# Performance work log

Measured on AMD Instinct MI355X. Metric: run time of the kernel, lower is better.

The kernel has to match this reference:

```python
import jax, jax.numpy as jnp
import numpy as np

B, C, H, W = 4, 512, 64, 64
CA = C // 2  # attention hidden channels


def _conv1x1(x, w):
    # w: [O, I], x: [B, I, H, W]
    return jnp.einsum('oi,bihw->bohw', w, x)


def _conv3x3(x, w, b):
    y = jax.lax.conv_general_dilated(x, w, (1, 1), 'SAME',
                                     dimension_numbers=('NCHW', 'OIHW', 'NCHW'))
    return y + b[None, :, None, None]


def _scan_dir(x, w, b, axis, reverse):
    # IRNN recurrence along `axis`: prev = relu(prev * w + b + x_t), per-channel w,b.
    # The boundary position (first in scan order after un-flipping) stays zero,
    # matching the torch code which never writes it.
    xs = jnp.moveaxis(x, axis, 0)          # [L, B, C, other]
    if reverse:
        xs = xs[::-1]
    wb = w.reshape(1, -1, 1)
    bb = b.reshape(1, -1, 1)

    def step(prev, xt):
        new = jax.nn.relu(prev * wb + bb + xt)
        return new, new

    init = jax.nn.relu(xs[0])
    _, ys = jax.lax.scan(step, init, xs[1:])
    ys = jnp.concatenate([jnp.zeros_like(ys[:1]), ys], axis=0)
    if reverse:
        ys = ys[::-1]
    return jnp.moveaxis(ys, 0, axis)


def _irnn(x, wu, wr, wd, wl, bu, br, bd, bl):
    up = _scan_dir(x, wu, bu, 2, True)     # scans from bottom row upward
    right = _scan_dir(x, wr, br, 3, False)
    down = _scan_dir(x, wd, bd, 2, False)
    left = _scan_dir(x, wl, bl, 3, True)
    return up, right, down, left


def setup_inputs() -> dict:
    key = jax.random.key(0)
    ks = jax.random.split(key, 32)

    def n(k, shape, scale):
        return jax.random.normal(k, shape, jnp.float32) * scale

    inp = {
        'x': n(ks[0], (B, C, H, W), 1.0),
        # Attention: conv3x3(C->C/2)+b, conv3x3(C/2->C/2)+b, conv1x1(C/2->4)+b
        'a_w1': n(ks[1], (CA, C, 3, 3), (C * 9) ** -0.5),
        'a_b1': n(ks[2], (CA,), 0.02),
        'a_w2': n(ks[3], (CA, CA, 3, 3), (CA * 9) ** -0.5),
        'a_b2': n(ks[4], (CA,), 0.02),
        'a_w3': n(ks[5], (4, CA, 1, 1), CA ** -0.5),
        'a_b3': n(ks[6], (4,), 0.02),
        'cin_w': n(ks[7], (C, C), C ** -0.5),   # conv_in 1x1, bias=False
        'c2_w': n(ks[8], (C, 4 * C), (4 * C) ** -0.5),
        'c3_w': n(ks[9], (C, 4 * C), (4 * C) ** -0.5),
    }
    # IRNN per-channel recurrence weights (alpha=1.0 init) and biases
    i = 10
    for tag in ('i1', 'i2'):
        for d in ('u', 'r', 'd', 'l'):
            inp[f'{tag}_w{d}'] = jnp.ones((C,), jnp.float32)
            inp[f'{tag}_b{d}'] = n(ks[i], (C,), 0.05)
            i += 1
    return inp


def reference(x, a_w1, a_b1, a_w2, a_b2, a_w3, a_b3, cin_w,
              i1_wu, i1_bu, i1_wr, i1_br, i1_wd, i1_bd, i1_wl, i1_bl,
              c2_w,
              i2_wu, i2_bu, i2_wr, i2_br, i2_wd, i2_bd, i2_wl, i2_bl,
              c3_w):
    # Attention branch — computed but NEVER applied: the original torch code
    # uses out-of-place .mul() and discards the result (faithful reproduction).
    a = jax.nn.relu(_conv3x3(x, a_w1, a_b1))
    a = jax.nn.relu(_conv3x3(a, a_w2, a_b2))
    _weight = jax.nn.sigmoid(_conv1x1(a, a_w3[:, :, 0, 0]) + a_b3[None, :, None, None])

    out = _conv1x1(x, cin_w)
    u, r, d, l = _irnn(out, i1_wu, i1_wr, i1_wd, i1_wl, i1_bu, i1_br, i1_bd, i1_bl)
    out = jnp.concatenate([u, r, d, l], axis=1)   # [B, 4C, H, W]
    out = _conv1x1(out, c2_w)
    u, r, d, l = _irnn(out, i2_wu, i2_wr, i2_wd, i2_wl, i2_bu, i2_br, i2_bd, i2_bl)
    out = jnp.concatenate([u, r, d, l], axis=1)
    out = jax.nn.relu(_conv1x1(out, c3_w))
    return out
```

## Files before the change

### kernel.cpp

```cpp
#include <hip/hip_runtime.h>
#include <stdint.h>

#define NB 4
#define CB 512
#define HH 64
#define WW 64
#define HW 4096
#define C4 2048
#define PTOT (NB*HW)

typedef float  f32x4  __attribute__((ext_vector_type(4)));
typedef short  bf16x8 __attribute__((ext_vector_type(8)));

__device__ __forceinline__ float relu_f(float v){ return v > 0.f ? v : 0.f; }

__device__ __forceinline__ float bf2f(unsigned short u){
    union { uint32_t i; float f; } v; v.i = ((uint32_t)u) << 16; return v.f;
}
__device__ __forceinline__ unsigned short f2bf(float f){
    union { float f; uint32_t i; } v; v.f = f;
    uint32_t r = v.i + 0x7FFFu + ((v.i >> 16) & 1u);
    return (unsigned short)(r >> 16);
}

__device__ __forceinline__ void gload16(const void* g, void* l){
    __builtin_amdgcn_global_load_lds(
        (const __attribute__((address_space(1))) uint32_t*)g,
        (__attribute__((address_space(3))) uint32_t*)l, 16, 0, 0);
}

__global__ __launch_bounds__(256) void cast3_f32_bf16(
    const float* __restrict__ a, unsigned short* __restrict__ oa,
    const float* __restrict__ b, unsigned short* __restrict__ ob,
    const float* __restrict__ c, unsigned short* __restrict__ oc)
{
    int i = blockIdx.x * 256 + threadIdx.x;
    const float* src; unsigned short* dst; int j;
    if (i < 65536)        { src = a; dst = oa; j = i; }
    else if (i < 327680)  { src = b; dst = ob; j = i - 65536; }
    else                  { src = c; dst = oc; j = i - 327680; }
    float4 v = ((const float4*)src)[j];
    ushort4 o;
    o.x = f2bf(v.x); o.y = f2bf(v.y); o.z = f2bf(v.z); o.w = f2bf(v.w);
    ((ushort4*)dst)[j] = o;
}

__global__ __launch_bounds__(256) void transpose_cast_x(
    const float* __restrict__ x, unsigned short* __restrict__ xT)
{
    __shared__ unsigned short tile[64][72];
    const int b  = blockIdx.z;
    const int p0 = blockIdx.x * 64;
    const int c0 = blockIdx.y * 64;
    const int t  = threadIdx.x;

    const int pl = (t & 15) * 4;
    const int cl = t >> 4;
    const float* src = x + ((size_t)b * CB + c0) * HW + p0;
    #pragma unroll
    for (int r = 0; r < 4; r++) {
        int c = cl + r * 16;
        float4 v = *(const float4*)(src + (size_t)c * HW + pl);
        tile[pl + 0][c] = f2bf(v.x);
        tile[pl + 1][c] = f2bf(v.y);
        tile[pl + 2][c] = f2bf(v.z);
        tile[pl + 3][c] = f2bf(v.w);
    }
    __syncthreads();
    unsigned short* dst = xT + ((size_t)b * HW + p0) * CB + c0;
    const int cl2 = (t & 15) * 4;
    const int pl2 = t >> 4;
    #pragma unroll
    for (int r = 0; r < 4; r++) {
        int p = pl2 + r * 16;
        ushort4 o = *(ushort4*)&tile[p][cl2];
        *(ushort4*)(dst + (size_t)p * CB + cl2) = o;
    }
}

template<int K, int OUTMODE>
__global__ __launch_bounds__(512) void gemm_cl(
    const unsigned short* __restrict__ A,
    const unsigned short* __restrict__ Bw,
    void* __restrict__ out)
{
    extern __shared__ __align__(16) char lds[];

    const int t    = threadIdx.x;
    const int lane = t & 63;
    const int wid  = t >> 6;
    const int p0   = blockIdx.x * 256;
    const int o0   = blockIdx.y * 128;

    const int l15 = lane & 15;
    const int l4  = lane >> 4;
    const int m0  = (wid >> 1) * 64;
    const int n0  = (wid & 1) * 64;
    const int swz = (l15 & 7) << 4;

    f32x4 acc[4][4];
    #pragma unroll
    for (int m = 0; m < 4; m++)
        #pragma unroll
        for (int n = 0; n < 4; n++) acc[m][n] = (f32x4)0.f;

    const int sr  = lane >> 3;
    const int scb = (lane & 7) * 16;
    const int skk = (scb ^ (sr << 4)) >> 1;

    auto STAGE_A = [&](int k0, int half, char* buf) {
        #pragma unroll
        for (int j = 0; j < 2; ++j) {
            const int r = half * 128 + j * 64 + wid * 8 + sr;
            gload16(A + (size_t)(p0 + r) * K + k0 + skk,
                    buf + half * 16384 + j * 8192 + wid * 1024);
        }
    };
    auto STAGE_B = [&](int k0, char* buf) {
        #pragma unroll
        for (int j = 0; j < 2; ++j) {
            const int r = j * 64 + wid * 8 + sr;
            gload16(Bw + (size_t)(o0 + r) * K + k0 + skk,
                    buf + 32768 + j * 8192 + wid * 1024);
        }
    };

    char* buf0 = lds;
    char* buf1 = lds + 49152;
    char* buf2 = lds + 98304;

    STAGE_A(0, 0, buf0); STAGE_A(0, 1, buf0); STAGE_B(0, buf0);
    STAGE_A(64, 0, buf1); STAGE_A(64, 1, buf1); STAGE_B(64, buf1);

    char* cur = buf0; char* nxt = buf1; char* fut = buf2;
    const int NT = K / 64;

#define PH(khv, mhv, STCODE)                                                   \
    {                                                                          \
        const int colb = (khv) * 64 + l4 * 16;                                 \
        af0 = *(const bf16x8*)(cur + (m0 + (2*(mhv)  )*16 + l15)*128 + (colb ^ swz)); \
        af1 = *(const bf16x8*)(cur + (m0 + (2*(mhv)+1)*16 + l15)*128 + (colb ^ swz)); \
        if ((mhv) == 0) {                                                      \
            _Pragma("unroll")                                                  \
            for (int nn = 0; nn < 4; ++nn)                                     \
                bfr[nn] = *(const bf16x8*)(cur + 32768 +                       \
                           (n0 + nn*16 + l15)*128 + (colb ^ swz));             \
        }                                                                      \
        STCODE;                                                                \
        __builtin_amdgcn_s_barrier();                                          \
        asm volatile("s_waitcnt lgkmcnt(0)" ::: "memory");                     \
        __builtin_amdgcn_sched_barrier(0);                                     \
        __builtin_amdgcn_s_setprio(1);                                         \
        _Pragma("unroll")                                                      \
        for (int nn = 0; nn < 4; ++nn) {                                       \
            acc[2*(mhv)  ][nn] = __builtin_amdgcn_mfma_f32_16x16x32_bf16(      \
                                    af0, bfr[nn], acc[2*(mhv)  ][nn], 0, 0, 0);\
            acc[2*(mhv)+1][nn] = __builtin_amdgcn_mfma_f32_16x16x32_bf16(      \
                                    af1, bfr[nn], acc[2*(mhv)+1][nn], 0, 0, 0);\
        }                                                                      \
        __builtin_amdgcn_s_setprio(0);                                         \
        __builtin_amdgcn_sched_barrier(0);                                     \
        __builtin_amdgcn_s_barrier();                                          \
    }

    for (int tt = 0; tt < NT; ++tt) {
        if (tt < NT - 1) asm volatile("s_waitcnt vmcnt(6)" ::: "memory");
        else             asm volatile("s_waitcnt vmcnt(0)" ::: "memory");
        __builtin_amdgcn_s_barrier();

        const int  k2 = (tt + 2) * 64;
        const bool st = (tt + 2 < NT);
        bf16x8 bfr[4], af0, af1;

        PH(0, 0, { if (st) STAGE_A(k2, 0, fut); })
        PH(0, 1, { if (st) STAGE_A(k2, 1, fut); })
        PH(1, 0, { if (st) STAGE_B(k2, fut);    })
        PH(1, 1, { })

        char* tmp = cur; cur = nxt; nxt = fut; fut = tmp;
    }
#undef PH

    if (OUTMODE == 0) {
        unsigned short* op = (unsigned short*)out;
        #pragma unroll
        for (int m = 0; m < 4; m++)
            #pragma unroll
            for (int r = 0; r < 4; r++) {
                const int p = p0 + m0 + m * 16 + l4 * 4 + r;
                #pragma unroll
                for (int n = 0; n < 4; n++) {
                    const int o = o0 + n0 + n * 16 + l15;
                    op[(size_t)p * CB + o] = f2bf(acc[m][n][r]);
                }
            }
    } else {
        __syncthreads();
        float (*tl)[260] = (float(*)[260])lds;
        #pragma unroll
        for (int n = 0; n < 4; n++)
            #pragma unroll
            for (int m = 0; m < 4; m++)
                #pragma unroll
                for (int r = 0; r < 4; r++)
                    tl[n0 + n * 16 + l15][m0 + m * 16 + l4 * 4 + r] = acc[m][n][r];
        __syncthreads();
        const int bb   = p0 >> 12;
        const int phw0 = p0 & (HW - 1);
        const int orow = t >> 2;
        const int pseg = (t & 3) * 64;
        float* dst = (float*)out + ((size_t)(bb * CB + o0 + orow)) * HW + phw0 + pseg;
        #pragma unroll
        for (int j = 0; j < 16; j++) {
            float4 v = *(float4*)&tl[orow][pseg + j * 4];
            v.x = relu_f(v.x); v.y = relu_f(v.y); v.z = relu_f(v.z); v.w = relu_f(v.w);
            *(float4*)(dst + j * 4) = v;
        }
    }
}

__global__ __launch_bounds__(256) void irnn_fused(
    const unsigned short* __restrict__ in, unsigned short* __restrict__ outc,
    const float* __restrict__ wu, const float* __restrict__ bu,
    const float* __restrict__ wr, const float* __restrict__ br,
    const float* __restrict__ wd, const float* __restrict__ bd,
    const float* __restrict__ wl, const float* __restrict__ bl)
{
    const int dir = blockIdx.y;
    const float* wv; const float* bv; int pstep, rev;
    if      (dir == 0) { wv = wu; bv = bu; pstep = 64; rev = 1; }
    else if (dir == 1) { wv = wr; bv = br; pstep = 1;  rev = 0; }
    else if (dir == 2) { wv = wd; bv = bd; pstep = 64; rev = 0; }
    else               { wv = wl; bv = bl; pstep = 1;  rev = 1; }
    const int dirOff = dir * 512;

    const int idx = blockIdx.x * 256 + threadIdx.x;
    const int c = idx & 511;
    const int f = (idx >> 9) & 63;
    const int b = idx >> 15;
    const int fbase = (pstep == 64) ? f : f * 64;

    const float wc = wv[c], bc = bv[c];
    const int t0 = rev ? 63 : 0;
    const int dp = rev ? -pstep : pstep;
    const int istep = dp * CB;
    const int ostep = dp * C4;

    const unsigned short* ip = in   + ((size_t)b * HW + fbase + (size_t)t0 * pstep) * CB + c;
    unsigned short*       op = outc + ((size_t)b * HW + fbase + (size_t)t0 * pstep) * C4 + dirOff + c;

    float s = relu_f(bf2f(ip[0]));
    op[0] = 0;

    unsigned short v0 = ip[1*istep], v1 = ip[2*istep], v2 = ip[3*istep], v3 = ip[4*istep],
                   v4 = ip[5*istep], v5 = ip[6*istep], v6 = ip[7*istep], v7 = ip[8*istep];

#define DO(kk, vv) { s = relu_f(fmaf(s, wc, bc + bf2f(vv))); op[(kk)*ostep] = f2bf(s); }
    for (int g = 0; g < 6; ++g) {
        const int k0 = 1 + 8 * g;
        DO(k0+0, v0); v0 = ip[(k0+ 8)*istep];
        DO(k0+1, v1); v1 = ip[(k0+ 9)*istep];
        DO(k0+2, v2); v2 = ip[(k0+10)*istep];
        DO(k0+3, v3); v3 = ip[(k0+11)*istep];
        DO(k0+4, v4); v4 = ip[(k0+12)*istep];
        DO(k0+5, v5); v5 = ip[(k0+13)*istep];
        DO(k0+6, v6); v6 = ip[(k0+14)*istep];
        DO(k0+7, v7); v7 = ip[(k0+15)*istep];
    }
    DO(49, v0); v0 = ip[57*istep];
    DO(50, v1); v1 = ip[58*istep];
    DO(51, v2); v2 = ip[59*istep];
    DO(52, v3); v3 = ip[60*istep];
    DO(53, v4); v4 = ip[61*istep];
    DO(54, v5); v5 = ip[62*istep];
    DO(55, v6); v6 = ip[63*istep];
    DO(56, v7);
    DO(57, v0); DO(58, v1); DO(59, v2); DO(60, v3);
    DO(61, v4); DO(62, v5); DO(63, v6);
#undef DO
}

extern "C" void kernel_launch(void* const* d_in, const int* in_sizes, int n_in,
                              void* d_out, int out_size, void* d_ws, size_t ws_size,
                              hipStream_t stream) {
    const float* x     = (const float*)d_in[0];
    const float* cin_w = (const float*)d_in[7];
    const float* c2_w  = (const float*)d_in[8];
    const float* c3_w  = (const float*)d_in[9];
    const float* i1_wu = (const float*)d_in[10];
    const float* i1_bu = (const float*)d_in[11];
    const float* i1_wr = (const float*)d_in[12];
    const float* i1_br = (const float*)d_in[13];
    const float* i1_wd = (const float*)d_in[14];
    const float* i1_bd = (const float*)d_in[15];
    const float* i1_wl = (const float*)d_in[16];
    const float* i1_bl = (const float*)d_in[17];
    const float* i2_wu = (const float*)d_in[18];
    const float* i2_bu = (const float*)d_in[19];
    const float* i2_wr = (const float*)d_in[20];
    const float* i2_br = (const float*)d_in[21];
    const float* i2_wd = (const float*)d_in[22];
    const float* i2_bd = (const float*)d_in[23];
    const float* i2_wl = (const float*)d_in[24];
    const float* i2_bl = (const float*)d_in[25];

    char* ws = (char*)d_ws;
    unsigned short* xT     = (unsigned short*)(ws);
    unsigned short* concat = (unsigned short*)(ws + (size_t)16 * 1024 * 1024);
    unsigned short* mid    = (unsigned short*)(ws + (size_t)80 * 1024 * 1024);
    unsigned short* wA     = (unsigned short*)(ws + (size_t)96 * 1024 * 1024);
    unsigned short* wB     = (unsigned short*)(wA + 512 * 512);
    unsigned short* wC     = (unsigned short*)(wB + 512 * 2048);

    cast3_f32_bf16<<<2304, 256, 0, stream>>>(cin_w, wA, c2_w, wB, c3_w, wC);
    transpose_cast_x<<<dim3(HW/64, CB/64, NB), 256, 0, stream>>>(x, xT);

    dim3 ggrid(PTOT/256, 4);
    dim3 sgrid(512, 4);
    const size_t GEMM_LDS = 147456;

    gemm_cl<512, 0><<<ggrid, 512, GEMM_LDS, stream>>>(xT, wA, mid);

    irnn_fused<<<sgrid, 256, 0, stream>>>(mid, concat,
        i1_wu, i1_bu, i1_wr, i1_br, i1_wd, i1_bd, i1_wl, i1_bl);

    gemm_cl<2048, 0><<<ggrid, 512, GEMM_LDS, stream>>>(concat, wB, mid);

    irnn_fused<<<sgrid, 256, 0, stream>>>(mid, concat,
        i2_wu, i2_bu, i2_wr, i2_br, i2_wd, i2_bd, i2_wl, i2_bl);

    gemm_cl<2048, 1><<<ggrid, 512, GEMM_LDS, stream>>>(concat, wC, d_out);
}
```

Before: 168.8 us.

## Retile GEMM to 128x256 blocks with double-buffered LDS pipeline

Measured after the change: 157.6 us. -6.6%, faster.

```diff
diff --git a/kernel.cpp b/kernel.cpp
--- a/kernel.cpp
+++ b/kernel.cpp
@@ -79,7 +79,8 @@
 }
 
 template<int K, int OUTMODE>
-__global__ __launch_bounds__(512) void gemm_cl(
+__global__ __launch_bounds__(512) __attribute__((amdgpu_waves_per_eu(1, 2)))
+void gemm_cl(
     const unsigned short* __restrict__ A,
     const unsigned short* __restrict__ Bw,
     void* __restrict__ out)
@@ -89,13 +90,13 @@
     const int t    = threadIdx.x;
     const int lane = t & 63;
     const int wid  = t >> 6;
-    const int p0   = blockIdx.x * 256;
-    const int o0   = blockIdx.y * 128;
+    const int p0   = blockIdx.x * 128;
+    const int o0   = blockIdx.y * 256;
 
     const int l15 = lane & 15;
     const int l4  = lane >> 4;
-    const int m0  = (wid >> 1) * 64;
-    const int n0  = (wid & 1) * 64;
+    const int wm  = (wid >> 2) * 64;
+    const int wn  = (wid & 3) * 64;
     const int swz = (l15 & 7) << 4;
 
     f32x4 acc[4][4];
@@ -108,45 +109,33 @@
     const int scb = (lane & 7) * 16;
     const int skk = (scb ^ (sr << 4)) >> 1;
 
-    auto STAGE_A = [&](int k0, int half, char* buf) {
-        #pragma unroll
-        for (int j = 0; j < 2; ++j) {
-            const int r = half * 128 + j * 64 + wid * 8 + sr;
-            gload16(A + (size_t)(p0 + r) * K + k0 + skk,
-                    buf + half * 16384 + j * 8192 + wid * 1024);
-        }
+    auto STAGE = [&](int k0, int bufo) {
+        #pragma unroll
+        for (int j = 0; j < 2; ++j)
+            gload16(A + (size_t)(p0 + j * 64 + wid * 8 + sr) * K + k0 + skk,
+                    lds + bufo + j * 8192 + wid * 1024);
+        #pragma unroll
+        for (int j = 0; j < 4; ++j)
+            gload16(Bw + (size_t)(o0 + j * 64 + wid * 8 + sr) * K + k0 + skk,
+                    lds + bufo + 16384 + j * 8192 + wid * 1024);
     };
-    auto STAGE_B = [&](int k0, char* buf) {
-        #pragma unroll
-        for (int j = 0; j < 2; ++j) {
-            const int r = j * 64 + wid * 8 + sr;
-            gload16(Bw + (size_t)(o0 + r) * K + k0 + skk,
-                    buf + 32768 + j * 8192 + wid * 1024);
-        }
-    };
-
-    char* buf0 = lds;
-    char* buf1 = lds + 49152;
-    char* buf2 = lds + 98304;
-
-    STAGE_A(0, 0, buf0); STAGE_A(0, 1, buf0); STAGE_B(0, buf0);
-    STAGE_A(64, 0, buf1); STAGE_A(64, 1, buf1); STAGE_B(64, buf1);
-
-    char* cur = buf0; char* nxt = buf1; char* fut = buf2;
+
+    STAGE(0, 0);
     const int NT = K / 64;
 
 #define PH(khv, mhv, STCODE)                                                   \
     {                                                                          \
         const int colb = (khv) * 64 + l4 * 16;                                 \
-        af0 = *(const bf16x8*)(cur + (m0 + (2*(mhv)  )*16 + l15)*128 + (colb ^ swz)); \
-        af1 = *(const bf16x8*)(cur + (m0 + (2*(mhv)+1)*16 + l15)*128 + (colb ^ swz)); \
+        af0 = *(const bf16x8*)(lds + co + (wm + (2*(mhv)  )*16 + l15)*128 + (colb ^ swz)); \
+        af1 = *(const bf16x8*)(lds + co + (wm + (2*(mhv)+1)*16 + l15)*128 + (colb ^ swz)); \
         if ((mhv) == 0) {                                                      \
             _Pragma("unroll")                                                  \
             for (int nn = 0; nn < 4; ++nn)                                     \
-                bfr[nn] = *(const bf16x8*)(cur + 32768 +                       \
-                           (n0 + nn*16 + l15)*128 + (colb ^ swz));             \
+                bfr[nn] = *(const bf16x8*)(lds + co + 16384 +                  \
+                           (wn + nn*16 + l15)*128 + (colb ^ swz));             \
         }                                                                      \
         STCODE;                                                                \
+        __builtin_amdgcn_sched_barrier(0);                                     \
         __builtin_amdgcn_s_barrier();                                          \
         asm volatile("s_waitcnt lgkmcnt(0)" ::: "memory");                     \
         __builtin_amdgcn_sched_barrier(0);                                     \
@@ -163,21 +152,20 @@
         __builtin_amdgcn_s_barrier();                                          \
     }
 
+    #pragma unroll 1
     for (int tt = 0; tt < NT; ++tt) {
-        if (tt < NT - 1) asm volatile("s_waitcnt vmcnt(6)" ::: "memory");
-        else             asm volatile("s_waitcnt vmcnt(0)" ::: "memory");
+        const int co = (tt & 1) * 49152;
+        const int no = 49152 - co;
+        asm volatile("s_waitcnt vmcnt(0)" ::: "memory");
         __builtin_amdgcn_s_barrier();
-
-        const int  k2 = (tt + 2) * 64;
-        const bool st = (tt + 2 < NT);
+        const bool st = (tt + 1 < NT);
+        const int k1 = (tt + 1) * 64;
         bf16x8 bfr[4], af0, af1;
 
-        PH(0, 0, { if (st) STAGE_A(k2, 0, fut); })
-        PH(0, 1, { if (st) STAGE_A(k2, 1, fut); })
-        PH(1, 0, { if (st) STAGE_B(k2, fut);    })
+        PH(0, 0, { if (st) STAGE(k1, no); })
+        PH(0, 1, { })
+        PH(1, 0, { })
         PH(1, 1, { })
-
-        char* tmp = cur; cur = nxt; nxt = fut; fut = tmp;
     }
 #undef PH
 
@@ -187,34 +175,42 @@
         for (int m = 0; m < 4; m++)
             #pragma unroll
             for (int r = 0; r < 4; r++) {
-                const int p = p0 + m0 + m * 16 + l4 * 4 + r;
+                const int p = p0 + wm + m * 16 + l4 * 4 + r;
                 #pragma unroll
                 for (int n = 0; n < 4; n++) {
-                    const int o = o0 + n0 + n * 16 + l15;
+                    const int o = o0 + wn + n * 16 + l15;
                     op[(size_t)p * CB + o] = f2bf(acc[m][n][r]);
                 }
             }
     } else {
         __syncthreads();
-        float (*tl)[260] = (float(*)[260])lds;
-        #pragma unroll
-        for (int n = 0; n < 4; n++)
-            #pragma unroll
-            for (int m = 0; m < 4; m++)
-                #pragma unroll
-                for (int r = 0; r < 4; r++)
-                    tl[n0 + n * 16 + l15][m0 + m * 16 + l4 * 4 + r] = acc[m][n][r];
-        __syncthreads();
+        float (*tl)[132] = (float(*)[132])lds;
         const int bb   = p0 >> 12;
         const int phw0 = p0 & (HW - 1);
-        const int orow = t >> 2;
-        const int pseg = (t & 3) * 64;
-        float* dst = (float*)out + ((size_t)(bb * CB + o0 + orow)) * HW + phw0 + pseg;
-        #pragma unroll
-        for (int j = 0; j < 16; j++) {
-            float4 v = *(float4*)&tl[orow][pseg + j * 4];
-            v.x = relu_f(v.x); v.y = relu_f(v.y); v.z = relu_f(v.z); v.w = relu_f(v.w);
-            *(float4*)(dst + j * 4) = v;
+        #pragma unroll
+        for (int h = 0; h < 2; ++h) {
+            if (((wid >> 1) & 1) == h) {
+                #pragma unroll
+                for (int n = 0; n < 4; n++)
+                    #pragma unroll
+                    for (int m = 0; m < 4; m++)
+                        #pragma unroll
+                        for (int r = 0; r < 4; r++)
+                            tl[(wn & 127) + n * 16 + l15][wm + m * 16 + l4 * 4 + r]
+                                = acc[m][n][r];
+            }
+            __syncthreads();
+            const int orow = t >> 2;
+            const int pseg = (t & 3) * 32;
+            float* dst = (float*)out +
+                ((size_t)(bb * CB + o0 + h * 128 + orow)) * HW + phw0 + pseg;
+            #pragma unroll
+            for (int j = 0; j < 8; j++) {
+                float4 v = *(float4*)&tl[orow][pseg + j * 4];
+                v.x = relu_f(v.x); v.y = relu_f(v.y); v.z = relu_f(v.z); v.w = relu_f(v.w);
+                *(float4*)(dst + j * 4) = v;
+            }
+            __syncthreads();
         }
     }
 }
@@ -315,9 +311,9 @@
     cast3_f32_bf16<<<2304, 256, 0, stream>>>(cin_w, wA, c2_w, wB, c3_w, wC);
     transpose_cast_x<<<dim3(HW/64, CB/64, NB), 256, 0, stream>>>(x, xT);
 
-    dim3 ggrid(PTOT/256, 4);
+    dim3 ggrid(PTOT/128, CB/256);
     dim3 sgrid(512, 4);
-    const size_t GEMM_LDS = 147456;
+    const size_t GEMM_LDS = 98304;
 
     gemm_cl<512, 0><<<ggrid, 512, GEMM_LDS, stream>>>(xT, wA, mid);
 
```
